# Kernel tuning notes

Measured on AMD Instinct MI355X. Metric: run time of the kernel, lower is better.

## Reference

```python
import jax, jax.numpy as jnp
import numpy as np

B, M, D = 256, 256, 16
H1, H2 = 64, 64
HN = H1 // 2  # split_half keeps first half as next-layer state


def setup_inputs() -> dict:
    key = jax.random.key(0)
    ks = jax.random.split(key, 8)
    x = jax.random.normal(ks[0], (B, M), dtype=jnp.float32)
    emb = 0.02 * jax.random.normal(ks[1], (M, D), dtype=jnp.float32)  # field_embedding
    # Conv1d(kernel=1) weights squeezed to [out_ch, in_ch]
    def xavier(k, o, i):
        lim = np.sqrt(6.0 / (o + i)).astype(np.float32)
        return jax.random.uniform(k, (o, i), dtype=jnp.float32, minval=-lim, maxval=lim)
    W0 = xavier(ks[2], H1, M * M)      # layer 0: in_ch = m*m
    b0 = jnp.zeros((H1,), dtype=jnp.float32)
    W1 = xavier(ks[3], H2, HN * M)     # layer 1: in_ch = (H1//2)*m
    b1 = jnp.zeros((H2,), dtype=jnp.float32)
    out_width = (H1 - HN) + H2         # 32 + 64 = 96
    fcW = xavier(ks[4], 2, out_width)
    fcb = jnp.zeros((2,), dtype=jnp.float32)
    return {"x": x, "emb": emb, "W0": W0, "b0": b0, "W1": W1, "b1": b1, "fcW": fcW, "fcb": fcb}


def _cin_layer(Xk_prev, X0, W, b):
    # outer product over fields, flattened: Z [B, prev_H*m, d]
    Bd = X0.shape[0]
    Z = jnp.einsum('bhd,bmd->bhmd', Xk_prev, X0).reshape(Bd, -1, X0.shape[-1])
    # kernel-1 Conv1d == channel-mixing matmul per d slice, + bias, + relu
    return jax.nn.relu(jnp.einsum('bcd,oc->bod', Z, W) + b[None, :, None])


def reference(x, emb, W0, b0, W1, b1, fcW, fcb):
    X0 = jnp.einsum('bi,ij->bij', x, emb)          # [B, m, d]
    X1 = _cin_layer(X0, X0, W0, b0)                # [B, H1, d]
    out1 = X1[:, HN:, :]                            # direct output half
    Xp = X1[:, :HN, :]                              # hidden half feeds next layer
    X2 = _cin_layer(Xp, X0, W1, b1)                # [B, H2, d] (last layer: full output)
    cin_out = jnp.concatenate([out1.sum(axis=2), X2.sum(axis=2)], axis=1)  # [B, 96]
    return cin_out @ fcW.T + fcb
```

## Files before the change

kernel.cpp:

```cpp
#include <hip/hip_runtime.h>

typedef unsigned short u16;
typedef short bf16x8 __attribute__((ext_vector_type(8)));
typedef float f32x4 __attribute__((ext_vector_type(4)));

#define AS1 __attribute__((address_space(1)))
#define AS3 __attribute__((address_space(3)))

__device__ __forceinline__ u16 f2bf(float f) {
    unsigned u = __float_as_uint(f);
    u += 0x7fffu + ((u >> 16) & 1u);
    return (u16)(u >> 16);
}
__device__ __forceinline__ float bf2f(u16 h) {
    return __uint_as_float(((unsigned)h) << 16);
}

__device__ __forceinline__ void gload_lds16(const void* g, void* l) {
    __builtin_amdgcn_global_load_lds((AS1 unsigned int*)(g),
                                     (AS3 unsigned int*)(l), 16, 0, 0);
}

__global__ void prep_kernel(const float* __restrict__ W0, const float* __restrict__ W1,
                            const float* __restrict__ x, const float* __restrict__ emb,
                            u16* __restrict__ W0b, u16* __restrict__ W1b,
                            u16* __restrict__ Qt, u16* __restrict__ E1) {
    int gid = blockIdx.x;
    if (gid < 4608) {
        int i = gid * 256 + threadIdx.x;
        const float* src; u16* dst; int j;
        if (i < 1048576) { src = W0; dst = W0b; j = i; }
        else             { src = W1; dst = W1b; j = i - 1048576; }
        float4 v = reinterpret_cast<const float4*>(src)[j];
        ushort4 o;
        o.x = f2bf(v.x); o.y = f2bf(v.y); o.z = f2bf(v.z); o.w = f2bf(v.w);
        reinterpret_cast<ushort4*>(dst)[j] = o;
    } else {
        int n = (gid - 4608) * 4 + (threadIdx.x >> 6);
        int lane = threadIdx.x & 63;
        int b = n >> 4, d = n & 15;
        int m0 = lane * 4;
        float4 xv = *reinterpret_cast<const float4*>(x + b * 256 + m0);
        ushort4 q;
        q.x = f2bf(xv.x * emb[(m0 + 0) * 16 + d]);
        q.y = f2bf(xv.y * emb[(m0 + 1) * 16 + d]);
        q.z = f2bf(xv.z * emb[(m0 + 2) * 16 + d]);
        q.w = f2bf(xv.w * emb[(m0 + 3) * 16 + d]);
        *reinterpret_cast<ushort4*>(Qt + n * 256 + m0) = q;
        int e1 = (n >> 8) * 65536 + (m0 >> 7) * 32768 + ((n >> 6) & 3) * 8192
               + ((m0 >> 4) & 7) * 1024 + ((n >> 4) & 3) * 256
               + (((m0 >> 2) & 3) * 16 + (n & 15)) * 4;
        *reinterpret_cast<ushort4*>(E1 + e1) = q;
    }
}

__global__ __launch_bounds__(512, 2) void cin1_kernel(
    const u16* __restrict__ W0b, const u16* __restrict__ Qt, const u16* __restrict__ E1,
    const float* __restrict__ b0, u16* __restrict__ E2, float* __restrict__ S1)
{
    __shared__ __attribute__((aligned(16))) u16 lds[2][2][2][8192];
    __shared__ float part[2][256];

    const int tid = threadIdx.x, lane = tid & 63, w = tid >> 6;
    const int wm = w >> 2, wn = w & 3;
    const int bid = blockIdx.x;
    const int o = (bid & 7) * 8 + ((bid >> 3) & 7);
    const int ntile = bid >> 6;

    const int srl = lane >> 3;
    const int ssw = ((lane & 7) ^ srl) * 8;
    const u16* aG = W0b + (o * 256 + w * 16 + srl) * 256 + ssw;
    const u16* bG = Qt + (ntile * 256 + w * 16 + srl) * 256 + ssw;
    const int ldsW = w * 1024;

    const int c15 = lane & 15;
    const int ph0s = (((lane >> 4) + 0) ^ (lane & 7)) * 8;
    const int ph1s = (((lane >> 4) + 4) ^ (lane & 7)) * 8;
    const u16* aB = &lds[0][0][wm][0] + c15 * 64;
    const u16* bB = &lds[0][1][wn >> 1][0] + (wn & 1) * 4096 + c15 * 64;

    f32x4 zero = {0.f, 0.f, 0.f, 0.f};
    f32x4 acc[8][4];
#pragma unroll
    for (int f = 0; f < 8; ++f)
#pragma unroll
        for (int g = 0; g < 4; ++g) acc[f][g] = zero;

    bf16x8 aR[4][2], bR[4][2];

#define STAGE(op, half, kt, buf)                                                          \
    {                                                                                     \
        const u16* s_ = (op) ? bG : aG;                                                   \
        gload_lds16(s_ + (half) * 32768 + (kt) * 64, &lds[buf][op][half][ldsW]);          \
        gload_lds16(s_ + (half) * 32768 + 2048 + (kt) * 64, &lds[buf][op][half][ldsW + 512]); \
    }
#define READ_A(buf, mh)                                                                   \
    _Pragma("unroll") for (int j_ = 0; j_ < 4; ++j_) {                                    \
        aR[j_][0] = *reinterpret_cast<const bf16x8*>(aB + (buf) * 32768 + ((mh) * 4 + j_) * 1024 + ph0s); \
        aR[j_][1] = *reinterpret_cast<const bf16x8*>(aB + (buf) * 32768 + ((mh) * 4 + j_) * 1024 + ph1s); \
    }
#define READ_B01(buf)                                                                     \
    _Pragma("unroll") for (int j_ = 0; j_ < 2; ++j_) {                                    \
        bR[j_][0] = *reinterpret_cast<const bf16x8*>(bB + (buf) * 32768 + j_ * 1024 + ph0s); \
        bR[j_][1] = *reinterpret_cast<const bf16x8*>(bB + (buf) * 32768 + j_ * 1024 + ph1s); \
    }
#define READ_B23(buf)                                                                     \
    _Pragma("unroll") for (int j_ = 0; j_ < 2; ++j_) {                                    \
        bR[2 + j_][0] = *reinterpret_cast<const bf16x8*>(bB + (buf) * 32768 + (2 + j_) * 1024 + ph0s); \
        bR[2 + j_][1] = *reinterpret_cast<const bf16x8*>(bB + (buf) * 32768 + (2 + j_) * 1024 + ph1s); \
    }
#define BARF() { __builtin_amdgcn_s_barrier(); asm volatile("" ::: "memory"); }
#define MFMA_Q(mh, nh)                                                                    \
    __builtin_amdgcn_sched_barrier(0);                                                    \
    __builtin_amdgcn_s_setprio(1);                                                        \
    _Pragma("unroll") for (int j_ = 0; j_ < 4; ++j_)                                      \
    _Pragma("unroll") for (int k_ = 0; k_ < 2; ++k_)                                      \
    _Pragma("unroll") for (int ks_ = 0; ks_ < 2; ++ks_)                                   \
        acc[(mh) * 4 + j_][(nh) * 2 + k_] = __builtin_amdgcn_mfma_f32_16x16x32_bf16(      \
            aR[j_][ks_], bR[(nh) * 2 + k_][ks_], acc[(mh) * 4 + j_][(nh) * 2 + k_], 0, 0, 0); \
    __builtin_amdgcn_s_setprio(0);                                                        \
    __builtin_amdgcn_sched_barrier(0);

    STAGE(0, 0, 0, 0) STAGE(0, 1, 0, 0) STAGE(1, 0, 0, 0) STAGE(1, 1, 0, 0)
    STAGE(0, 0, 1, 1) STAGE(0, 1, 1, 1) STAGE(1, 0, 1, 1) STAGE(1, 1, 1, 1)
    asm volatile("s_waitcnt vmcnt(8)" ::: "memory");
    BARF();

    READ_A(0, 0) READ_B01(0)                         BARF(); MFMA_Q(0, 0) BARF();
    READ_B23(0)                                      BARF(); MFMA_Q(0, 1) BARF();
    READ_A(0, 1) STAGE(1, 0, 2, 0)                   BARF(); MFMA_Q(1, 1) BARF();
    STAGE(1, 1, 2, 0) STAGE(0, 0, 2, 0)
    asm volatile("s_waitcnt vmcnt(6)" ::: "memory");
    BARF(); MFMA_Q(1, 0) BARF();
    READ_A(1, 0) READ_B01(1) STAGE(0, 1, 2, 0)       BARF(); MFMA_Q(0, 0) BARF();
    READ_B23(1)                                      BARF(); MFMA_Q(0, 1) BARF();
    READ_A(1, 1)                                     BARF(); MFMA_Q(1, 1) BARF();
    asm volatile("s_waitcnt vmcnt(0)" ::: "memory");
    BARF(); MFMA_Q(1, 0) BARF();

    READ_A(0, 0) READ_B01(0) STAGE(0, 0, 3, 1) STAGE(0, 1, 3, 1) BARF(); MFMA_Q(0, 0) BARF();
    READ_B23(0) STAGE(1, 0, 3, 1) STAGE(1, 1, 3, 1)              BARF(); MFMA_Q(0, 1) BARF();
    READ_A(0, 1)                                                 BARF(); MFMA_Q(1, 1) BARF();
    asm volatile("s_waitcnt vmcnt(0)" ::: "memory");
    BARF(); MFMA_Q(1, 0) BARF();
    READ_A(1, 0) READ_B01(1)                                     BARF(); MFMA_Q(0, 0) BARF();
    READ_B23(1)                                                  BARF(); MFMA_Q(0, 1) BARF();
    READ_A(1, 1)                                                 BARF(); MFMA_Q(1, 1) BARF();
    BARF(); MFMA_Q(1, 0)

#undef STAGE
#undef READ_A
#undef READ_B01
#undef READ_B23
#undef MFMA_Q

    float psum[4] = {0.f, 0.f, 0.f, 0.f};
    const u16* eb = E1 + ntile * 65536 + wm * 32768 + wn * 8192 + lane * 4;
#pragma unroll
    for (int f = 0; f < 8; ++f)
#pragma unroll
        for (int g = 0; g < 4; ++g) {
            ushort4 wv = *reinterpret_cast<const ushort4*>(eb + f * 1024 + g * 256);
            psum[g] += bf2f(wv.x) * acc[f][g][0] + bf2f(wv.y) * acc[f][g][1]
                     + bf2f(wv.z) * acc[f][g][2] + bf2f(wv.w) * acc[f][g][3];
        }
#pragma unroll
    for (int g = 0; g < 4; ++g) {
        float p = psum[g];
        p += __shfl_xor(p, 16);
        p += __shfl_xor(p, 32);
        if (lane < 16) part[wm][wn * 64 + g * 16 + lane] = p;
    }
    __syncthreads();
    if (tid < 256) {
        const int nl = tid;
        float v = part[0][nl] + part[1][nl] + b0[o];
        float r = fmaxf(v, 0.0f);
        const int n = ntile * 256 + nl;
        if (o < 32) {
            E2[(n >> 4) * 512 + (n & 15) * 32 + o] = f2bf(r);
        } else {
            float s = r;
            s += __shfl_xor(s, 1); s += __shfl_xor(s, 2);
            s += __shfl_xor(s, 4); s += __shfl_xor(s, 8);
            if ((n & 15) == 0) S1[(n >> 4) * 32 + (o - 32)] = s;
        }
    }
}

__global__ __launch_bounds__(256, 4) void cin2_kernel(
    const u16* __restrict__ W1b, const u16* __restrict__ Qt, const u16* __restrict__ E2,
    const float* __restrict__ b1, float* __restrict__ S2)
{
    __shared__ __attribute__((aligned(16))) u16 As[3][4096];
    __shared__ __attribute__((aligned(16))) u16 Bs[3][4096];
    __shared__ float part[2][2][128];

    const int tid = threadIdx.x, lane = tid & 63, w = tid >> 6;
    const int wh = w >> 1, wn = w & 1;
    const int bid = blockIdx.x;
    const int g8 = bid & 7, rest = bid >> 3;
    const int og = g8 * 2 + (rest & 1);
    const int ntile = rest >> 1;

    const int rl = lane >> 2;
    const int sw = ((lane & 3) ^ ((rl + (rl >> 2)) & 3)) << 3;
    const u16* aS0 = W1b + (og * 128 + (w * 2 + 0) * 16 + rl) * 256 + sw;
    const u16* aS1 = W1b + (og * 128 + (w * 2 + 1) * 16 + rl) * 256 + sw;
    const u16* bS0 = Qt + (ntile * 128 + (w * 2 + 0) * 16 + rl) * 256 + sw;
    const u16* bS1 = Qt + (ntile * 128 + (w * 2 + 1) * 16 + rl) * 256 + sw;
    const int ldsI0 = (w * 2 + 0) * 512, ldsI1 = (w * 2 + 1) * 512;

    const int rbA = wh * 64 + (lane & 15);
    const int rbB = wn * 64 + (lane & 15);
    const int sl = lane >> 4;
    const int aOff = rbA * 32 + ((sl ^ ((rbA + (rbA >> 2)) & 3)) << 3);
    const int bOff = rbB * 32 + ((sl ^ ((rbB + (rbB >> 2)) & 3)) << 3);

    f32x4 zero = {0.f, 0.f, 0.f, 0.f};
    f32x4 acc[4][4];
#pragma unroll
    for (int f = 0; f < 4; ++f)
#pragma unroll
        for (int gg = 0; gg < 4; ++gg) acc[f][gg] = zero;

    auto stage = [&](int kc, int bb) {
        int ko = kc * 32;
        gload_lds16(aS0 + ko, &As[bb][ldsI0]);
        gload_lds16(aS1 + ko, &As[bb][ldsI1]);
        gload_lds16(bS0 + ko, &Bs[bb][ldsI0]);
        gload_lds16(bS1 + ko, &Bs[bb][ldsI1]);
    };

    stage(0, 0); stage(1, 1);
#pragma unroll
    for (int kc = 0; kc < 8; ++kc) {
        if (kc < 7) asm volatile("s_waitcnt vmcnt(4)" ::: "memory");
        else        asm volatile("s_waitcnt vmcnt(0)" ::: "memory");
        __builtin_amdgcn_s_barrier();
        asm volatile("" ::: "memory");
        if (kc < 6) stage(kc + 2, (kc + 2) % 3);
        const u16* Ab = &As[kc % 3][0];
        const u16* Bb = &Bs[kc % 3][0];
        bf16x8 a[4], b[4];
#pragma unroll
        for (int f = 0; f < 4; ++f)
            a[f] = *reinterpret_cast<const bf16x8*>(Ab + aOff + f * 512);
#pragma unroll
        for (int gg = 0; gg < 4; ++gg)
            b[gg] = *reinterpret_cast<const bf16x8*>(Bb + bOff + gg * 512);
        __builtin_amdgcn_s_setprio(1);
#pragma unroll
        for (int f = 0; f < 4; ++f)
#pragma unroll
            for (int gg = 0; gg < 4; ++gg)
                acc[f][gg] = __builtin_amdgcn_mfma_f32_16x16x32_bf16(a[f], b[gg], acc[f][gg], 0, 0, 0);
        __builtin_amdgcn_s_setprio(0);
    }

    float psum[2][4] = {{0.f,0.f,0.f,0.f},{0.f,0.f,0.f,0.f}};
    const u16* eb = E2 + (ntile * 2 + wn) * 2048 + (lane & 15) * 32 + (lane >> 4) * 4;
#pragma unroll
    for (int f = 0; f < 4; ++f)
#pragma unroll
        for (int gg = 0; gg < 4; ++gg) {
            ushort4 wv = *reinterpret_cast<const ushort4*>(eb + gg * 512 + (f & 1) * 16);
            psum[f >> 1][gg] += bf2f(wv.x) * acc[f][gg][0] + bf2f(wv.y) * acc[f][gg][1]
                              + bf2f(wv.z) * acc[f][gg][2] + bf2f(wv.w) * acc[f][gg][3];
        }
#pragma unroll
    for (int ol = 0; ol < 2; ++ol)
#pragma unroll
        for (int gg = 0; gg < 4; ++gg) {
            float p = psum[ol][gg];
            p += __shfl_xor(p, 16);
            p += __shfl_xor(p, 32);
            if (lane < 16) part[wh][ol][wn * 64 + gg * 16 + lane] = p;
        }
    __syncthreads();
    if (tid < 128) {
        const int nl = tid;
        const int n = ntile * 128 + nl;
#pragma unroll
        for (int o4 = 0; o4 < 4; ++o4) {
            const int oo = og * 4 + o4;
            float v = part[o4 >> 1][o4 & 1][nl] + b1[oo];
            float r = fmaxf(v, 0.0f);
            float s = r;
            s += __shfl_xor(s, 1); s += __shfl_xor(s, 2);
            s += __shfl_xor(s, 4); s += __shfl_xor(s, 8);
            if ((nl & 15) == 0) S2[(n >> 4) * 64 + oo] = s;
        }
    }
}

__global__ void final_fc_kernel(const float* __restrict__ S1, const float* __restrict__ S2,
                                const float* __restrict__ fcW, const float* __restrict__ fcb,
                                float* __restrict__ out) {
    int b = threadIdx.x;
    float a0 = fcb[0], a1 = fcb[1];
#pragma unroll 8
    for (int c = 0; c < 32; ++c) {
        float v = S1[b * 32 + c];
        a0 += v * fcW[c]; a1 += v * fcW[96 + c];
    }
#pragma unroll 8
    for (int c = 0; c < 64; ++c) {
        float v = S2[b * 64 + c];
        a0 += v * fcW[32 + c]; a1 += v * fcW[96 + 32 + c];
    }
    out[b * 2 + 0] = a0;
    out[b * 2 + 1] = a1;
}

extern "C" void kernel_launch(void* const* d_in, const int* in_sizes, int n_in,
                              void* d_out, int out_size, void* d_ws, size_t ws_size,
                              hipStream_t stream) {
    const float* x   = (const float*)d_in[0];
    const float* emb = (const float*)d_in[1];
    const float* W0  = (const float*)d_in[2];
    const float* b0  = (const float*)d_in[3];
    const float* W1  = (const float*)d_in[4];
    const float* b1  = (const float*)d_in[5];
    const float* fcW = (const float*)d_in[6];
    const float* fcb = (const float*)d_in[7];
    float* out = (float*)d_out;

    char* ws = (char*)d_ws;
    u16*   W0b = (u16*)(ws);
    u16*   W1b = (u16*)(ws + 8388608);
    u16*   Qt  = (u16*)(ws + 9437184);
    u16*   E1  = (u16*)(ws + 11534336);
    u16*   E2  = (u16*)(ws + 13631488);
    float* S1  = (float*)(ws + 13893632);
    float* S2  = (float*)(ws + 13926400);

    prep_kernel<<<5632, 256, 0, stream>>>(W0, W1, x, emb, W0b, W1b, Qt, E1);
    cin1_kernel<<<1024, 512, 0, stream>>>(W0b, Qt, E1, b0, E2, S1);
    cin2_kernel<<<512, 256, 0, stream>>>(W1b, Qt, E2, b1, S2);
    final_fc_kernel<<<1, 256, 0, stream>>>(S1, S2, fcW, fcb, out);
}
```

Before: 73.75 us.

## Load A operand directly from global and stage only B through registers

Replaces the hand-scheduled global_load_lds double-buffered pipeline for both operands with a simpler loop. The A operand (W0) is now read straight from global memory into registers per MFMA fragment, and only B goes through LDS via a register-staged double buffer. LDS use and barrier count drop, and launch bounds change from 2 to 1 blocks per CU, freeing registers. The risk is that A is no longer shared through LDS, so each wave issues more global loads. The loss of fine-grained interleaving and lower occupancy may also expose latency.

```diff
diff --git a/kernel.cpp b/kernel.cpp
--- a/kernel.cpp
+++ b/kernel.cpp
@@ -54,11 +54,11 @@
     }
 }
 
-__global__ __launch_bounds__(512, 2) void cin1_kernel(
+__global__ __launch_bounds__(512, 1) void cin1_kernel(
     const u16* __restrict__ W0b, const u16* __restrict__ Qt, const u16* __restrict__ E1,
     const float* __restrict__ b0, u16* __restrict__ E2, float* __restrict__ S1)
 {
-    __shared__ __attribute__((aligned(16))) u16 lds[2][2][2][8192];
+    __shared__ __attribute__((aligned(16))) u16 Bs[2][16384];
     __shared__ float part[2][256];
 
     const int tid = threadIdx.x, lane = tid & 63, w = tid >> 6;
@@ -67,17 +67,17 @@
     const int o = (bid & 7) * 8 + ((bid >> 3) & 7);
     const int ntile = bid >> 6;
 
-    const int srl = lane >> 3;
-    const int ssw = ((lane & 7) ^ srl) * 8;
-    const u16* aG = W0b + (o * 256 + w * 16 + srl) * 256 + ssw;
-    const u16* bG = Qt + (ntile * 256 + w * 16 + srl) * 256 + ssw;
-    const int ldsW = w * 1024;
-
-    const int c15 = lane & 15;
-    const int ph0s = (((lane >> 4) + 0) ^ (lane & 7)) * 8;
-    const int ph1s = (((lane >> 4) + 4) ^ (lane & 7)) * 8;
-    const u16* aB = &lds[0][0][wm][0] + c15 * 64;
-    const u16* bB = &lds[0][1][wn >> 1][0] + (wn & 1) * 4096 + c15 * 64;
+    const int sc8 = tid & 7;
+    const int sr0 = tid >> 3;
+    const u16* bSrc = Qt + (ntile * 256 + sr0) * 256 + sc8 * 8;
+    const int sLds = sr0 * 64 + ((sc8 ^ (sr0 & 7)) * 8);
+
+    const u16* aBase = W0b + (o * 256 + wm * 128 + (lane & 15)) * 256 + (lane >> 4) * 8;
+
+    const int bn0 = wn * 64 + (lane & 15);
+    const int bq = lane >> 4;
+    const int bOffs0 = bn0 * 64 + (((0 + bq) ^ (bn0 & 7)) * 8);
+    const int bOffs1 = bn0 * 64 + (((4 + bq) ^ (bn0 & 7)) * 8);
 
     f32x4 zero = {0.f, 0.f, 0.f, 0.f};
     f32x4 acc[8][4];
@@ -86,73 +86,53 @@
 #pragma unroll
         for (int g = 0; g < 4; ++g) acc[f][g] = zero;
 
-    bf16x8 aR[4][2], bR[4][2];
-
-#define STAGE(op, half, kt, buf)                                                          \
-    {                                                                                     \
-        const u16* s_ = (op) ? bG : aG;                                                   \
-        gload_lds16(s_ + (half) * 32768 + (kt) * 64, &lds[buf][op][half][ldsW]);          \
-        gload_lds16(s_ + (half) * 32768 + 2048 + (kt) * 64, &lds[buf][op][half][ldsW + 512]); \
-    }
-#define READ_A(buf, mh)                                                                   \
-    _Pragma("unroll") for (int j_ = 0; j_ < 4; ++j_) {                                    \
-        aR[j_][0] = *reinterpret_cast<const bf16x8*>(aB + (buf) * 32768 + ((mh) * 4 + j_) * 1024 + ph0s); \
-        aR[j_][1] = *reinterpret_cast<const bf16x8*>(aB + (buf) * 32768 + ((mh) * 4 + j_) * 1024 + ph1s); \
-    }
-#define READ_B01(buf)                                                                     \
-    _Pragma("unroll") for (int j_ = 0; j_ < 2; ++j_) {                                    \
-        bR[j_][0] = *reinterpret_cast<const bf16x8*>(bB + (buf) * 32768 + j_ * 1024 + ph0s); \
-        bR[j_][1] = *reinterpret_cast<const bf16x8*>(bB + (buf) * 32768 + j_ * 1024 + ph1s); \
-    }
-#define READ_B23(buf)                                                                     \
-    _Pragma("unroll") for (int j_ = 0; j_ < 2; ++j_) {                                    \
-        bR[2 + j_][0] = *reinterpret_cast<const bf16x8*>(bB + (buf) * 32768 + (2 + j_) * 1024 + ph0s); \
-        bR[2 + j_][1] = *reinterpret_cast<const bf16x8*>(bB + (buf) * 32768 + (2 + j_) * 1024 + ph1s); \
-    }
-#define BARF() { __builtin_amdgcn_s_barrier(); asm volatile("" ::: "memory"); }
-#define MFMA_Q(mh, nh)                                                                    \
-    __builtin_amdgcn_sched_barrier(0);                                                    \
-    __builtin_amdgcn_s_setprio(1);                                                        \
-    _Pragma("unroll") for (int j_ = 0; j_ < 4; ++j_)                                      \
-    _Pragma("unroll") for (int k_ = 0; k_ < 2; ++k_)                                      \
-    _Pragma("unroll") for (int ks_ = 0; ks_ < 2; ++ks_)                                   \
-        acc[(mh) * 4 + j_][(nh) * 2 + k_] = __builtin_amdgcn_mfma_f32_16x16x32_bf16(      \
-            aR[j_][ks_], bR[(nh) * 2 + k_][ks_], acc[(mh) * 4 + j_][(nh) * 2 + k_], 0, 0, 0); \
-    __builtin_amdgcn_s_setprio(0);                                                        \
-    __builtin_amdgcn_sched_barrier(0);
-
-    STAGE(0, 0, 0, 0) STAGE(0, 1, 0, 0) STAGE(1, 0, 0, 0) STAGE(1, 1, 0, 0)
-    STAGE(0, 0, 1, 1) STAGE(0, 1, 1, 1) STAGE(1, 0, 1, 1) STAGE(1, 1, 1, 1)
-    asm volatile("s_waitcnt vmcnt(8)" ::: "memory");
-    BARF();
-
-    READ_A(0, 0) READ_B01(0)                         BARF(); MFMA_Q(0, 0) BARF();
-    READ_B23(0)                                      BARF(); MFMA_Q(0, 1) BARF();
-    READ_A(0, 1) STAGE(1, 0, 2, 0)                   BARF(); MFMA_Q(1, 1) BARF();
-    STAGE(1, 1, 2, 0) STAGE(0, 0, 2, 0)
-    asm volatile("s_waitcnt vmcnt(6)" ::: "memory");
-    BARF(); MFMA_Q(1, 0) BARF();
-    READ_A(1, 0) READ_B01(1) STAGE(0, 1, 2, 0)       BARF(); MFMA_Q(0, 0) BARF();
-    READ_B23(1)                                      BARF(); MFMA_Q(0, 1) BARF();
-    READ_A(1, 1)                                     BARF(); MFMA_Q(1, 1) BARF();
-    asm volatile("s_waitcnt vmcnt(0)" ::: "memory");
-    BARF(); MFMA_Q(1, 0) BARF();
-
-    READ_A(0, 0) READ_B01(0) STAGE(0, 0, 3, 1) STAGE(0, 1, 3, 1) BARF(); MFMA_Q(0, 0) BARF();
-    READ_B23(0) STAGE(1, 0, 3, 1) STAGE(1, 1, 3, 1)              BARF(); MFMA_Q(0, 1) BARF();
-    READ_A(0, 1)                                                 BARF(); MFMA_Q(1, 1) BARF();
-    asm volatile("s_waitcnt vmcnt(0)" ::: "memory");
-    BARF(); MFMA_Q(1, 0) BARF();
-    READ_A(1, 0) READ_B01(1)                                     BARF(); MFMA_Q(0, 0) BARF();
-    READ_B23(1)                                                  BARF(); MFMA_Q(0, 1) BARF();
-    READ_A(1, 1)                                                 BARF(); MFMA_Q(1, 1) BARF();
-    BARF(); MFMA_Q(1, 0)
-
-#undef STAGE
-#undef READ_A
-#undef READ_B01
-#undef READ_B23
-#undef MFMA_Q
+    {
+        bf16x8 Breg[4];
+#pragma unroll
+        for (int i = 0; i < 4; ++i)
+            Breg[i] = *reinterpret_cast<const bf16x8*>(bSrc + i * 16384);
+#pragma unroll
+        for (int i = 0; i < 4; ++i)
+            *reinterpret_cast<bf16x8*>(&Bs[0][sLds + i * 4096]) = Breg[i];
+    }
+    asm volatile("s_waitcnt lgkmcnt(0)" ::: "memory");
+    __builtin_amdgcn_s_barrier();
+    asm volatile("" ::: "memory");
+
+#pragma unroll
+    for (int kt = 0; kt < 4; ++kt) {
+        const int cur = kt & 1;
+        bf16x8 Breg[4];
+        if (kt < 3) {
+#pragma unroll
+            for (int i = 0; i < 4; ++i)
+                Breg[i] = *reinterpret_cast<const bf16x8*>(bSrc + (kt + 1) * 64 + i * 16384);
+        }
+        bf16x8 bF[4][2];
+#pragma unroll
+        for (int fn = 0; fn < 4; ++fn) {
+            bF[fn][0] = *reinterpret_cast<const bf16x8*>(&Bs[cur][bOffs0 + fn * 1024]);
+            bF[fn][1] = *reinterpret_cast<const bf16x8*>(&Bs[cur][bOffs1 + fn * 1024]);
+        }
+#pragma unroll
+        for (int fm = 0; fm < 8; ++fm) {
+            bf16x8 a0 = *reinterpret_cast<const bf16x8*>(aBase + fm * 4096 + kt * 64);
+            bf16x8 a1 = *reinterpret_cast<const bf16x8*>(aBase + fm * 4096 + kt * 64 + 32);
+#pragma unroll
+            for (int fn = 0; fn < 4; ++fn) {
+                acc[fm][fn] = __builtin_amdgcn_mfma_f32_16x16x32_bf16(a0, bF[fn][0], acc[fm][fn], 0, 0, 0);
+                acc[fm][fn] = __builtin_amdgcn_mfma_f32_16x16x32_bf16(a1, bF[fn][1], acc[fm][fn], 0, 0, 0);
+            }
+        }
+        if (kt < 3) {
+#pragma unroll
+            for (int i = 0; i < 4; ++i)
+                *reinterpret_cast<bf16x8*>(&Bs[cur ^ 1][sLds + i * 4096]) = Breg[i];
+            asm volatile("s_waitcnt lgkmcnt(0)" ::: "memory");
+            __builtin_amdgcn_s_barrier();
+            asm volatile("" ::: "memory");
+        }
+    }
 
     float psum[4] = {0.f, 0.f, 0.f, 0.f};
     const u16* eb = E1 + ntile * 65536 + wm * 32768 + wn * 8192 + lane * 4;
```

Result: slower. 110.5 us (+49.9%).
